# Kernel optimization log

Hardware: AMD Instinct MI355X
Metric: run time of the kernel (lower is better)

Reference implementation:

```python
import jax, jax.numpy as jnp
import numpy as np
from jax import lax

STRIDE = 1
PAD = 1
KH = KW = 3


def conv2d(x, w, b=None, stride=STRIDE, pad=PAD):
    out = lax.conv_general_dilated(x, w, (stride, stride), [(pad, pad), (pad, pad)],
                                   dimension_numbers=("NCHW", "OIHW", "NCHW"))
    if b is not None:
        out = out + b[None, :, None, None]
    return out


def deform_conv2d(x, offset, mask, weight, stride=STRIDE, pad=PAD):
    """torchvision.ops.deform_conv2d (v2, single group) semantics."""
    B, C, H, W = x.shape
    Co, Ci, Kh, Kw = weight.shape
    K2 = Kh * Kw
    Ho = (H + 2 * pad - Kh) // stride + 1
    Wo = (W + 2 * pad - Kw) // stride + 1

    off = offset.reshape(B, K2, 2, Ho, Wo)  # [...,0]=dy, [...,1]=dx (row-major kernel order)
    ky = (jnp.arange(K2) // Kw).astype(x.dtype)
    kx = (jnp.arange(K2) % Kw).astype(x.dtype)
    hs = (jnp.arange(Ho) * stride - pad).astype(x.dtype)
    ws = (jnp.arange(Wo) * stride - pad).astype(x.dtype)

    # sampling coords [B, K2, Ho, Wo]
    py = off[:, :, 0] + hs[None, None, :, None] + ky[None, :, None, None]
    px = off[:, :, 1] + ws[None, None, None, :] + kx[None, :, None, None]

    y0 = jnp.floor(py)
    x0 = jnp.floor(px)
    wy1 = py - y0
    wx1 = px - x0
    wy0 = 1.0 - wy1
    wx0 = 1.0 - wx1
    y0i = y0.astype(jnp.int32)
    x0i = x0.astype(jnp.int32)

    xf = x.reshape(B, C, H * W)

    def gather(yi, xi):
        valid = (yi >= 0) & (yi < H) & (xi >= 0) & (xi < W)
        lin = jnp.clip(yi, 0, H - 1) * W + jnp.clip(xi, 0, W - 1)  # [B,K2,Ho,Wo]
        linf = lin.reshape(B, 1, -1)
        g = jnp.take_along_axis(xf, jnp.broadcast_to(linf, (B, C, linf.shape[-1])), axis=2)
        g = g.reshape(B, C, K2, Ho, Wo)
        return g * valid[:, None].astype(x.dtype)

    # bilinear combine, modulated by mask; v: [B, C, K2, Ho, Wo]
    v = ((wy0 * wx0)[:, None] * gather(y0i, x0i)
         + (wy0 * wx1)[:, None] * gather(y0i, x0i + 1)
         + (wy1 * wx0)[:, None] * gather(y0i + 1, x0i)
         + (wy1 * wx1)[:, None] * gather(y0i + 1, x0i + 1))
    v = v * mask[:, None]

    return jnp.einsum('bckhw,ock->bohw', v, weight.reshape(Co, Ci, K2))


def setup_inputs() -> dict:
    key = jax.random.key(0)
    ks = jax.random.split(key, 6)
    B, C, H, W = 2, 256, 64, 64
    Co = 256
    fan = C * KH * KW
    return {
        "x": jax.random.normal(ks[0], (B, C, H, W), jnp.float32),
        "residual": jax.random.normal(ks[1], (B, C, H, W), jnp.float32),
        "offset_w": jax.random.normal(ks[2], (2 * KH * KW, C, KH, KW), jnp.float32) * np.sqrt(2.0 / fan),
        "offset_b": jnp.zeros((2 * KH * KW,), jnp.float32),
        "mod_w": jax.random.normal(ks[3], (KH * KW, C, KH, KW), jnp.float32) * np.sqrt(2.0 / fan),
        "mod_b": jnp.zeros((KH * KW,), jnp.float32),
        "reg_w": jax.random.normal(ks[4], (Co, C, KH, KW), jnp.float32) * np.sqrt(2.0 / fan),
    }


def reference(x, residual, offset_w, offset_b, mod_w, mod_b, reg_w):
    offset = conv2d(residual, offset_w, offset_b)
    modulator = 2.0 * jax.nn.sigmoid(conv2d(x, mod_w, mod_b))
    return deform_conv2d(x, offset, modulator, reg_w)
```

## Files before the change

kernel.cpp:

```cpp
#include <hip/hip_runtime.h>
#include <hip/hip_bf16.h>
#include <math.h>

#define BB 2
#define CC 256
#define HH 64
#define WW 64
#define COo 256
#define HWs 4096
#define K2 9
#define CK 2304

typedef __attribute__((ext_vector_type(4))) float floatx4;
typedef __attribute__((ext_vector_type(8))) short shortx8;

#define O_WBF   221184
#define O_WPK   516096
#define O_XT    10027008
#define O_RT    11075584

__device__ __forceinline__ void gll16(const __hip_bfloat16* g, __hip_bfloat16* l) {
    __builtin_amdgcn_global_load_lds(
        (const __attribute__((address_space(1))) unsigned int*)g,
        (__attribute__((address_space(3))) unsigned int*)l, 16, 0, 0);
}

__device__ __forceinline__ short f2bf(float v) {
    __hip_bfloat16 h = __float2bfloat16(v);
    return *reinterpret_cast<short*>(&h);
}

__device__ __forceinline__ float bf2f(short s) {
    unsigned u = ((unsigned)(unsigned short)s) << 16;
    return __builtin_bit_cast(float, u);
}

__global__ __launch_bounds__(256) void prep_kernel(
    const float* __restrict__ x,
    const float* __restrict__ residual,
    const float* __restrict__ reg_w,
    const float* __restrict__ off_w,
    const float* __restrict__ mod_w,
    __hip_bfloat16* __restrict__ xT,
    __hip_bfloat16* __restrict__ resT,
    __hip_bfloat16* __restrict__ Wbf,
    __hip_bfloat16* __restrict__ Wpk)
{
    int blk = blockIdx.x;
    int t = threadIdx.x;
    if (blk < 2048) {
        int sel = blk >> 10;
        int bk  = blk & 1023;
        int oc = bk & 7;
        int y  = (bk >> 3) & 63;
        int b  = bk >> 9;
        int wo = t & 63;
        int cg = t >> 6;
        int c0 = oc * 32 + cg * 8;
        const float* src = (sel ? residual : x)
                           + ((size_t)(b * CC + c0) * HH + y) * WW + wo;
        shortx8 pk;
#pragma unroll
        for (int j = 0; j < 8; ++j) pk[j] = f2bf(src[(size_t)j * HWs]);
        __hip_bfloat16* dst = sel ? resT : xT;
        *(shortx8*)(dst + ((size_t)b * 4096 + y * 64 + wo) * 256 + c0) = pk;
    } else {
        int idx = (blk - 2048) * 256 + t;
        if (idx < CK * COo) {
            int co = idx / CK;
            int r  = idx - co * CK;
            int k  = r >> 8;
            int c  = r & 255;
            Wbf[idx] = __float2bfloat16(reg_w[(size_t)co * CK + c * 9 + k]);
        }
        if (idx < 147456) {
            int g    = idx / 73728;
            int rem  = idx % 73728;
            int kc   = rem / 9216;
            int r2   = rem % 9216;
            int tap  = r2 / 1024;
            int r3   = r2 & 1023;
            int nf   = r3 >> 9;
            int r4   = r3 & 511;
            int lane = r4 >> 3;
            int j    = r4 & 7;
            int c    = kc * 32 + (lane >> 4) * 8 + j;
            int n    = nf * 16 + (lane & 15);
            float v = 0.f;
            if (g == 0) { if (n < 18) v = off_w[((size_t)n * CC + c) * 9 + tap]; }
            else        { if (n < 9)  v = mod_w[((size_t)n * CC + c) * 9 + tap]; }
            Wpk[idx] = __float2bfloat16(v);
        }
    }
}

__global__ __launch_bounds__(1024) void mega_kernel(
    const __hip_bfloat16* __restrict__ xT,
    const __hip_bfloat16* __restrict__ resT,
    const __hip_bfloat16* __restrict__ Wpk,
    const float* __restrict__ off_b,
    const float* __restrict__ mod_b,
    const __hip_bfloat16* __restrict__ Wbf,
    float* __restrict__ out)
{
    int blk0 = blockIdx.x;
    int mt = ((blk0 & 7) << 5) | (blk0 >> 3);
    int t  = threadIdx.x;
    int lane = t & 63;
    int w    = t >> 6;
    int quad = lane >> 4;
    int ln   = lane & 15;
    int wm = w & 1;
    int wN = w >> 1;

    __shared__ __hip_bfloat16 As[2][32 * 64];
    __shared__ __hip_bfloat16 Bs[2][256 * 64];
    __shared__ int   s_mi[32][K2][4];
    __shared__ float s_mw[32][K2][4];
    __shared__ float s_out[16][16 * 20];
    __shared__ float s_off[32][18];
    __shared__ float s_msk[32][9];

    int b = mt >> 7;
    const __hip_bfloat16* xb = xT + (size_t)b * 4096 * 256;

    int lr8 = lane >> 3;
    int sub = lane & 7;
    int chk = sub ^ lr8;

    const __hip_bfloat16* gB = Wbf + (size_t)(w * 16 + lr8) * CK + chk * 8;

    floatx4 acc[2];
#pragma unroll
    for (int nf = 0; nf < 2; ++nf) acc[nf] = (floatx4){0.f, 0.f, 0.f, 0.f};

#pragma unroll
    for (int h = 0; h < 2; ++h)
        gll16(gB + (size_t)(h * 8) * CK, &Bs[0][w * 1024 + h * 512]);

    {
        int cg  = w >> 3;
        int wr  = w & 7;
        int cph = wr & 1;
        int cks = wr >> 1;
        const __hip_bfloat16* csrc = (cg ? xT : resT) + (size_t)b * 4096 * 256;
        const __hip_bfloat16* cwg  = Wpk + (size_t)cg * 73728
                                         + (size_t)cks * 2 * 9216;
        int cpix = (mt & 127) * 32 + cph * 16 + ln;
        int cho = cpix >> 6, cwo = cpix & 63;

        floatx4 ca0 = (floatx4){0.f, 0.f, 0.f, 0.f};
        floatx4 ca1 = (floatx4){0.f, 0.f, 0.f, 0.f};

        if (cg == 0) {
#pragma unroll
            for (int tap = 0; tap < 9; ++tap) {
                int ky = tap / 3, kx = tap % 3;
                int r  = cho + ky - 1;
                int cx = cwo + kx - 1;
                bool v = (r >= 0) && (r < HH) && (cx >= 0) && (cx < WW);
                int hw = v ? (r * WW + cx) : 0;
                const __hip_bfloat16* abase = csrc + (size_t)hw * 256
                                              + quad * 8 + cks * 64;
                const __hip_bfloat16* wbase = cwg + (size_t)tap * 1024 + lane * 8;
#pragma unroll
                for (int kc = 0; kc < 2; ++kc) {
                    shortx8 af = *(const shortx8*)(abase + kc * 32);
                    if (!v) {
                        shortx8 zf = {0,0,0,0,0,0,0,0};
                        af = zf;
                    }
                    shortx8 b0 = *(const shortx8*)(wbase + (size_t)kc * 9216);
                    shortx8 b1 = *(const shortx8*)(wbase + (size_t)kc * 9216 + 512);
                    ca0 = __builtin_amdgcn_mfma_f32_16x16x32_bf16(af, b0, ca0, 0, 0, 0);
                    ca1 = __builtin_amdgcn_mfma_f32_16x16x32_bf16(af, b1, ca1, 0, 0, 0);
                }
            }
        } else {
#pragma unroll
            for (int tap = 0; tap < 9; ++tap) {
                int ky = tap / 3, kx = tap % 3;
                int r  = cho + ky - 1;
                int cx = cwo + kx - 1;
                bool v = (r >= 0) && (r < HH) && (cx >= 0) && (cx < WW);
                int hw = v ? (r * WW + cx) : 0;
                const __hip_bfloat16* abase = csrc + (size_t)hw * 256
                                              + quad * 8 + cks * 64;
                const __hip_bfloat16* wbase = cwg + (size_t)tap * 1024 + lane * 8;
#pragma unroll
                for (int kc = 0; kc < 2; ++kc) {
                    shortx8 af = *(const shortx8*)(abase + kc * 32);
                    if (!v) {
                        shortx8 zf = {0,0,0,0,0,0,0,0};
                        af = zf;
                    }
                    shortx8 b0 = *(const shortx8*)(wbase + (size_t)kc * 9216);
                    ca0 = __builtin_amdgcn_mfma_f32_16x16x32_bf16(af, b0, ca0, 0, 0, 0);
                }
            }
        }

        float* s_red = (float*)&Bs[1][0];
        *(floatx4*)&s_red[((size_t)w * 64 + lane) * 8]     = ca0;
        *(floatx4*)&s_red[((size_t)w * 64 + lane) * 8 + 4] = ca1;
    }
    __syncthreads();

    {
        int cg = w >> 3;
        int wr = w & 7;
        if (wr < 2) {
            float* s_red = (float*)&Bs[1][0];
            floatx4 a0, a1;
#pragma unroll
            for (int j = 0; j < 4; ++j) {
                int base = cg * 8 + wr;
                a0[j] = s_red[(((size_t)base     * 64 + lane)) * 8 + j]
                      + s_red[(((size_t)(base+2) * 64 + lane)) * 8 + j]
                      + s_red[(((size_t)(base+4) * 64 + lane)) * 8 + j]
                      + s_red[(((size_t)(base+6) * 64 + lane)) * 8 + j];
                a1[j] = s_red[(((size_t)base     * 64 + lane)) * 8 + 4 + j]
                      + s_red[(((size_t)(base+2) * 64 + lane)) * 8 + 4 + j]
                      + s_red[(((size_t)(base+4) * 64 + lane)) * 8 + 4 + j]
                      + s_red[(((size_t)(base+6) * 64 + lane)) * 8 + 4 + j];
            }
#pragma unroll
            for (int nf = 0; nf < 2; ++nf) {
                floatx4 a = nf ? a1 : a0;
                int n = nf * 16 + ln;
#pragma unroll
                for (int i2 = 0; i2 < 4; ++i2) {
                    int p = wr * 16 + quad * 4 + i2;
                    if (cg == 0) {
                        if (n < 18)
                            s_off[p][n] = a[i2] + off_b[n];
                    } else {
                        if (n < 9) {
                            float z = a[i2] + mod_b[n];
                            s_msk[p][n] = 2.f / (1.f + __expf(-z));
                        }
                    }
                }
            }
        }
    }
    __syncthreads();

    for (int u = t; u < 32 * K2; u += 1024) {
        int pl_ = u / K2;
        int k  = u - pl_ * K2;
        int hw = (mt & 127) * 32 + pl_;
        int ho = hw >> 6, wo = hw & 63;
        float dy = s_off[pl_][2 * k];
        float dx = s_off[pl_][2 * k + 1];
        float m  = s_msk[pl_][k];
        float py = (float)(ho - 1 + k / 3) + dy;
        float px = (float)(wo - 1 + k % 3) + dx;
        float y0f = floorf(py), x0f = floorf(px);
        float wy1 = py - y0f, wx1 = px - x0f;
        float wy0 = 1.f - wy1, wx0 = 1.f - wx1;
        int y0 = (int)y0f, x0 = (int)x0f;
#pragma unroll
        for (int j = 0; j < 4; ++j) {
            int yy = y0 + (j >> 1);
            int xx = x0 + (j & 1);
            float wj = ((j == 0) ? wy0 * wx0 :
                        (j == 1) ? wy0 * wx1 :
                        (j == 2) ? wy1 * wx0 : wy1 * wx1) * m;
            bool valid = (yy >= 0) && (yy < HH) && (xx >= 0) && (xx < WW);
            s_mi[pl_][k][j] = valid ? (yy * WW + xx) : 0;
            s_mw[pl_][k][j] = valid ? wj : 0.f;
        }
    }

    int pl  = (t >> 3) & 31;
    int ch8 = t & 7;
    bool gth = (t < 256);
    int aslot = pl * 64 + ((ch8 ^ (pl & 7)) * 8);

    int   mi0, mi1, mi2, mi3;
    float mw0, mw1, mw2, mw3;
    auto meta_load = [&](int k) {
        mi0 = s_mi[pl][k][0]; mi1 = s_mi[pl][k][1];
        mi2 = s_mi[pl][k][2]; mi3 = s_mi[pl][k][3];
        mw0 = s_mw[pl][k][0]; mw1 = s_mw[pl][k][1];
        mw2 = s_mw[pl][k][2]; mw3 = s_mw[pl][k][3];
    };

    shortx8 gc0, gc1, gc2, gc3;
    float   gw0, gw1, gw2, gw3;
    auto gather_load = [&](int cb) {
        const __hip_bfloat16* xr = xb + cb * 64 + ch8 * 8;
        gc0 = *(const shortx8*)(xr + (size_t)mi0 * 256);
        gc1 = *(const shortx8*)(xr + (size_t)mi1 * 256);
        gc2 = *(const shortx8*)(xr + (size_t)mi2 * 256);
        gc3 = *(const shortx8*)(xr + (size_t)mi3 * 256);
        gw0 = mw0; gw1 = mw1; gw2 = mw2; gw3 = mw3;
    };
    auto gather_store = [&](int buf) {
        shortx8 o;
#pragma unroll
        for (int j = 0; j < 8; ++j)
            o[j] = f2bf(gw0 * bf2f(gc0[j]) + gw1 * bf2f(gc1[j])
                      + gw2 * bf2f(gc2[j]) + gw3 * bf2f(gc3[j]));
        *(shortx8*)&As[buf][aslot] = o;
    };

    __syncthreads();
    if (gth) {
        meta_load(0);
        gather_load(0);
        gather_store(0);
        gather_load(1);
    }

    int swz = ln & 7;

    for (int kt = 0; kt < 36; ++kt) {
        int cur = kt & 1;
        int nxt = cur ^ 1;
        __syncthreads();
        if (kt + 1 < 36) {
            int ko = (kt + 1) * 64;
#pragma unroll
            for (int h = 0; h < 2; ++h)
                gll16(gB + (size_t)(h * 8) * CK + ko, &Bs[nxt][w * 1024 + h * 512]);
        }
#pragma unroll
        for (int kh = 0; kh < 2; ++kh) {
            int slot = ((kh * 4 + quad) ^ swz) * 8;
            shortx8 af = *(const shortx8*)
                &As[cur][(wm * 16 + ln) * 64 + slot];
            shortx8 bf[2];
#pragma unroll
            for (int nf = 0; nf < 2; ++nf)
                bf[nf] = *(const shortx8*)
                    &Bs[cur][(wN * 32 + nf * 16 + ln) * 64 + slot];
#pragma unroll
            for (int nf = 0; nf < 2; ++nf)
                acc[nf] = __builtin_amdgcn_mfma_f32_16x16x32_bf16(
                    af, bf[nf], acc[nf], 0, 0, 0);
        }
        if (gth && kt + 1 < 36) gather_store(nxt);
        if (gth && kt + 2 < 36) {
            int k2 = kt + 2;
            if ((k2 & 3) == 0) meta_load(k2 >> 2);
            gather_load(k2 & 3);
        }
    }

    int bb = mt >> 7;
    int hw0 = (mt & 127) * 32 + wm * 16;
    float* sw = &s_out[w][0];
    int co_l = lane >> 2;
    int seg  = lane & 3;
#pragma unroll
    for (int nf = 0; nf < 2; ++nf) {
        *(floatx4*)&sw[ln * 20 + quad * 4] = acc[nf];
        floatx4 v0 = *(const floatx4*)&sw[co_l * 20 + seg * 4];
        int co = wN * 32 + nf * 16 + co_l;
        float* orow = out + ((size_t)(bb * COo + co) << 12) + hw0;
        *(floatx4*)&orow[seg * 4] = v0;
    }
}

extern "C" void kernel_launch(void* const* d_in, const int* in_sizes, int n_in,
                              void* d_out, int out_size, void* d_ws, size_t ws_size,
                              hipStream_t stream)
{
    const float* x     = (const float*)d_in[0];
    const float* resid = (const float*)d_in[1];
    const float* off_w = (const float*)d_in[2];
    const float* off_b = (const float*)d_in[3];
    const float* mod_w = (const float*)d_in[4];
    const float* mod_b = (const float*)d_in[5];
    const float* reg_w = (const float*)d_in[6];
    float* out = (float*)d_out;

    float* ws = (float*)d_ws;
    __hip_bfloat16* Wbf  = (__hip_bfloat16*)(ws + O_WBF);
    __hip_bfloat16* Wpk  = (__hip_bfloat16*)(ws + O_WPK);
    __hip_bfloat16* xT   = (__hip_bfloat16*)(ws + O_XT);
    __hip_bfloat16* resT = (__hip_bfloat16*)(ws + O_RT);

    prep_kernel<<<2048 + (CK * COo + 255) / 256, 256, 0, stream>>>(
        x, resid, reg_w, off_w, mod_w, xT, resT, Wbf, Wpk);

    mega_kernel<<<256, 1024, 0, stream>>>(xT, resT, Wpk, off_b, mod_b, Wbf, out);
}
```

Measured before the change: 127.2 us.

## Split output channels across two blocks to double grid size

Each block now computes 128 of the 256 output channels for its 32-pixel tile, and the grid doubles to 512 blocks. The B-tile shared buffer is halved, and each wave issues one MFMA per k-half instead of two. This aims to raise CU occupancy and parallelism. The cost is that the offset/modulator convolution and the deformable gather are recomputed redundantly by both blocks covering the same pixels.

```diff
diff --git a/kernel.cpp b/kernel.cpp
--- a/kernel.cpp
+++ b/kernel.cpp
@@ -104,7 +104,9 @@
     float* __restrict__ out)
 {
     int blk0 = blockIdx.x;
-    int mt = ((blk0 & 7) << 5) | (blk0 >> 3);
+    int blk = ((blk0 & 7) << 6) | (blk0 >> 3);
+    int nt = blk & 1;
+    int mt = blk >> 1;
     int t  = threadIdx.x;
     int lane = t & 63;
     int w    = t >> 6;
@@ -114,7 +116,7 @@
     int wN = w >> 1;
 
     __shared__ __hip_bfloat16 As[2][32 * 64];
-    __shared__ __hip_bfloat16 Bs[2][256 * 64];
+    __shared__ __hip_bfloat16 Bs[2][128 * 64];
     __shared__ int   s_mi[32][K2][4];
     __shared__ float s_mw[32][K2][4];
     __shared__ float s_out[16][16 * 20];
@@ -128,15 +130,9 @@
     int sub = lane & 7;
     int chk = sub ^ lr8;
 
-    const __hip_bfloat16* gB = Wbf + (size_t)(w * 16 + lr8) * CK + chk * 8;
-
-    floatx4 acc[2];
-#pragma unroll
-    for (int nf = 0; nf < 2; ++nf) acc[nf] = (floatx4){0.f, 0.f, 0.f, 0.f};
-
-#pragma unroll
-    for (int h = 0; h < 2; ++h)
-        gll16(gB + (size_t)(h * 8) * CK, &Bs[0][w * 1024 + h * 512]);
+    const __hip_bfloat16* gB = Wbf + (size_t)(nt * 128 + w * 8 + lr8) * CK + chk * 8;
+
+    floatx4 acc = (floatx4){0.f, 0.f, 0.f, 0.f};
 
     {
         int cg  = w >> 3;
@@ -200,7 +196,7 @@
             }
         }
 
-        float* s_red = (float*)&Bs[1][0];
+        float* s_red = (float*)&Bs[0][0];
         *(floatx4*)&s_red[((size_t)w * 64 + lane) * 8]     = ca0;
         *(floatx4*)&s_red[((size_t)w * 64 + lane) * 8 + 4] = ca1;
     }
@@ -210,7 +206,7 @@
         int cg = w >> 3;
         int wr = w & 7;
         if (wr < 2) {
-            float* s_red = (float*)&Bs[1][0];
+            float* s_red = (float*)&Bs[0][0];
             floatx4 a0, a1;
 #pragma unroll
             for (int j = 0; j < 4; ++j) {
@@ -245,6 +241,8 @@
         }
     }
     __syncthreads();
+
+    gll16(gB, &Bs[0][w * 512]);
 
     for (int u = t; u < 32 * K2; u += 1024) {
         int pl_ = u / K2;
@@ -322,24 +320,16 @@
         __syncthreads();
         if (kt + 1 < 36) {
             int ko = (kt + 1) * 64;
-#pragma unroll
-            for (int h = 0; h < 2; ++h)
-                gll16(gB + (size_t)(h * 8) * CK + ko, &Bs[nxt][w * 1024 + h * 512]);
+            gll16(gB + ko, &Bs[nxt][w * 512]);
         }
 #pragma unroll
         for (int kh = 0; kh < 2; ++kh) {
             int slot = ((kh * 4 + quad) ^ swz) * 8;
             shortx8 af = *(const shortx8*)
                 &As[cur][(wm * 16 + ln) * 64 + slot];
-            shortx8 bf[2];
-#pragma unroll
-            for (int nf = 0; nf < 2; ++nf)
-                bf[nf] = *(const shortx8*)
-                    &Bs[cur][(wN * 32 + nf * 16 + ln) * 64 + slot];
-#pragma unroll
-            for (int nf = 0; nf < 2; ++nf)
-                acc[nf] = __builtin_amdgcn_mfma_f32_16x16x32_bf16(
-                    af, bf[nf], acc[nf], 0, 0, 0);
+            shortx8 bf = *(const shortx8*)
+                &Bs[cur][(wN * 16 + ln) * 64 + slot];
+            acc = __builtin_amdgcn_mfma_f32_16x16x32_bf16(af, bf, acc, 0, 0, 0);
         }
         if (gth && kt + 1 < 36) gather_store(nxt);
         if (gth && kt + 2 < 36) {
@@ -354,11 +344,10 @@
     float* sw = &s_out[w][0];
     int co_l = lane >> 2;
     int seg  = lane & 3;
-#pragma unroll
-    for (int nf = 0; nf < 2; ++nf) {
-        *(floatx4*)&sw[ln * 20 + quad * 4] = acc[nf];
+    {
+        *(floatx4*)&sw[ln * 20 + quad * 4] = acc;
         floatx4 v0 = *(const floatx4*)&sw[co_l * 20 + seg * 4];
-        int co = wN * 32 + nf * 16 + co_l;
+        int co = nt * 128 + wN * 16 + co_l;
         float* orow = out + ((size_t)(bb * COo + co) << 12) + hw0;
         *(floatx4*)&orow[seg * 4] = v0;
     }
@@ -386,5 +375,5 @@
     prep_kernel<<<2048 + (CK * COo + 255) / 256, 256, 0, stream>>>(
         x, resid, reg_w, off_w, mod_w, xT, resT, Wbf, Wpk);
 
-    mega_kernel<<<256, 1024, 0, stream>>>(xT, resT, Wpk, off_b, mod_b, Wbf, out);
-}
+    mega_kernel<<<512, 1024, 0, stream>>>(xT, resT, Wpk, off_b, mod_b, Wbf, out);
+}
```

Measured after the change: 155.3 us. 1.22x slower.
